# Optimization experiments

Measured on AMD Instinct MI355X. Metric: run time of the kernel, lower is better.

The kernel has to match this reference:

```python
import jax, jax.numpy as jnp
import numpy as np

N_NODES = 100000
N_EDGES = 1600000
D_IN, D_HID, D_OUT = 128, 128, 64


def setup_inputs() -> dict:
    key = jax.random.key(0)
    k1, k2, k3, k4 = jax.random.split(key, 4)
    x = jax.random.normal(k1, (N_NODES, D_IN), dtype=jnp.float32)
    edge_index = jax.random.randint(k2, (2, N_EDGES), 0, N_NODES, dtype=jnp.int64)
    # Glorot-style weights, zero bias (GCNConv defaults: weight + bias)
    W1 = jax.random.normal(k3, (D_IN, D_HID), dtype=jnp.float32) * (1.0 / np.sqrt(D_IN))
    b1 = jnp.zeros((D_HID,), dtype=jnp.float32)
    W2 = jax.random.normal(k4, (D_HID, D_OUT), dtype=jnp.float32) * (1.0 / np.sqrt(D_HID))
    b2 = jnp.zeros((D_OUT,), dtype=jnp.float32)
    return {"x": x, "edge_index": edge_index, "W1": W1, "b1": b1, "W2": W2, "b2": b2}


def reference(x, edge_index, W1, b1, W2, b2):
    n = x.shape[0]
    src, dst = edge_index[0], edge_index[1]
    # GCN symmetric normalization, add_self_loops=False
    ones = jnp.ones((src.shape[0],), dtype=x.dtype)
    deg = jax.ops.segment_sum(ones, dst, num_segments=n)
    deg_inv_sqrt = jnp.where(deg > 0, jax.lax.rsqrt(jnp.maximum(deg, 1.0)), 0.0)
    norm = deg_inv_sqrt[src] * deg_inv_sqrt[dst]  # [E]

    def gcn_conv(h, W, b):
        h = h @ W                                   # [N, d_out] transform first
        msg = h[src] * norm[:, None]                # [E, d_out] gather + scale
        agg = jax.ops.segment_sum(msg, dst, num_segments=n)  # scatter-add
        return agg + b

    h = jax.nn.relu(gcn_conv(x, W1, b1))
    # dropout(p=0.6) is identity in eval mode (training=False)
    return gcn_conv(h, W2, b2)
```

## Files before the change

kernel.cpp:

```cpp
#include <hip/hip_runtime.h>

#define N_NODES 100000
#define N_EDGES 1600000
#define NBUCK 391
#define CHUNKA 8192
#define NBLKA 196

typedef __bf16 bf16x8 __attribute__((ext_vector_type(8)));
typedef float f32x4 __attribute__((ext_vector_type(4)));

__device__ inline unsigned short bf1(float a) {
    unsigned u = __builtin_bit_cast(unsigned, a);
    u = (u + 0x7FFF + ((u >> 16) & 1)) >> 16;
    return (unsigned short)u;
}
__device__ inline unsigned bfpack(float a, float b) {
    unsigned ua = __builtin_bit_cast(unsigned, a);
    unsigned ub = __builtin_bit_cast(unsigned, b);
    ua = (ua + 0x7FFF + ((ua >> 16) & 1)) >> 16;
    ub = (ub + 0x7FFF + ((ub >> 16) & 1)) >> 16;
    return ua | (ub << 16);
}
__device__ inline float bf2f(unsigned short u) {
    return __builtin_bit_cast(float, ((unsigned)u) << 16);
}
__device__ inline float bflo(unsigned v) { return __builtin_bit_cast(float, v << 16); }
__device__ inline float bfhi(unsigned v) { return __builtin_bit_cast(float, v & 0xFFFF0000u); }

__global__ __launch_bounds__(256) void bhist_kernel(const int* __restrict__ ei,
                                                    int* __restrict__ bhist) {
    __shared__ int hist[NBUCK];
    const int t = threadIdx.x;
    const int e0 = blockIdx.x * CHUNKA;
    const int n  = min(CHUNKA, N_EDGES - e0);
    for (int i = t; i < NBUCK; i += 256) hist[i] = 0;
    __syncthreads();
    for (int i = t; i < n; i += 256) {
        int dst = ei[N_EDGES + e0 + i];
        atomicAdd(&hist[dst >> 8], 1);
    }
    __syncthreads();
    for (int i = t; i < NBUCK; i += 256)
        if (hist[i]) atomicAdd(&bhist[i], hist[i]);
}

__global__ __launch_bounds__(512) void prep_kernel(const int* __restrict__ bhist,
                                                   int* __restrict__ boffs,
                                                   const float* __restrict__ W1,
                                                   const float* __restrict__ W2,
                                                   unsigned short* __restrict__ Wt1,
                                                   unsigned short* __restrict__ Wt2) {
    const int t = threadIdx.x;
    if (blockIdx.x == 0) {
        __shared__ int s[512];
        int v = (t < NBUCK) ? bhist[t] : 0;
        s[t] = v;
        __syncthreads();
#pragma unroll
        for (int off = 1; off < 512; off <<= 1) {
            int tv = (t >= off) ? s[t - off] : 0;
            __syncthreads();
            s[t] += tv;
            __syncthreads();
        }
        if (t < NBUCK) boffs[t] = s[t] - v;
        if (t == NBUCK - 1) boffs[NBUCK] = s[t];
    } else if (blockIdx.x == 1) {
        for (int i = t; i < 128 * 128; i += 512) {
            int k = i >> 7, n = i & 127;
            Wt1[n * 128 + k] = bf1(W1[i]);
        }
    } else {
        for (int i = t; i < 128 * 64; i += 512) {
            int k = i >> 6, n = i & 63;
            Wt2[n * 128 + k] = bf1(W2[i]);
        }
    }
}

__global__ __launch_bounds__(256) void binA_kernel(const int* __restrict__ ei,
                                                   const int* __restrict__ boffs,
                                                   int* __restrict__ bcur,
                                                   unsigned* __restrict__ epk) {
    __shared__ int hist[NBUCK], base[NBUCK], cur[NBUCK];
    const int t = threadIdx.x;
    const int e0 = blockIdx.x * CHUNKA;
    const int n  = min(CHUNKA, N_EDGES - e0);
    for (int i = t; i < NBUCK; i += 256) hist[i] = 0;
    __syncthreads();
    for (int i = t; i < n; i += 256) {
        int dst = ei[N_EDGES + e0 + i];
        atomicAdd(&hist[dst >> 8], 1);
    }
    __syncthreads();
    for (int i = t; i < NBUCK; i += 256) {
        int h = hist[i];
        base[i] = boffs[i] + (h ? atomicAdd(&bcur[i], h) : 0);
        cur[i]  = 0;
    }
    __syncthreads();
    for (int i = t; i < n; i += 256) {
        int src = ei[e0 + i];
        int dst = ei[N_EDGES + e0 + i];
        int b   = dst >> 8;
        int r   = atomicAdd(&cur[b], 1);
        epk[base[b] + r] = ((unsigned)src << 8) | (unsigned)(dst & 255);
    }
}

__global__ __launch_bounds__(256) void binB_kernel(const unsigned* __restrict__ epk,
                                                   const int* __restrict__ boffs,
                                                   int* __restrict__ deg,
                                                   float* __restrict__ dis,
                                                   int* __restrict__ offs,
                                                   int* __restrict__ srcn) {
    __shared__ int cnt[256], s[256], loff[256];
    const int b  = blockIdx.x;
    const int t  = threadIdx.x;
    const int n0 = b << 8;
    const int base = boffs[b];
    const int end  = boffs[b + 1];
    cnt[t] = 0;
    __syncthreads();
    for (int e = base + t; e < end; e += 256)
        atomicAdd(&cnt[epk[e] & 255u], 1);
    __syncthreads();
    int v = cnt[t];
    s[t] = v;
    __syncthreads();
#pragma unroll
    for (int off = 1; off < 256; off <<= 1) {
        int tv = (t >= off) ? s[t - off] : 0;
        __syncthreads();
        s[t] += tv;
        __syncthreads();
    }
    loff[t] = s[t] - v;
    {
        int node = n0 + t;
        if (node < N_NODES) {
            deg[node]  = v;
            dis[node]  = (v > 0) ? rsqrtf((float)v) : 0.0f;
            offs[node] = base + loff[t];
        }
    }
    cnt[t] = 0;
    __syncthreads();
    for (int e = base + t; e < end; e += 256) {
        unsigned p = epk[e];
        int li  = (int)(p & 255u);
        int r   = atomicAdd(&cnt[li], 1);
        srcn[base + loff[li] + r] = (int)(p >> 8);
    }
}

__global__ __launch_bounds__(256) void gemm1_kernel(const float* __restrict__ x,
                                                    const unsigned short* __restrict__ Wt1,
                                                    const float* __restrict__ dis,
                                                    unsigned short* __restrict__ h1b) {
    __shared__ unsigned short Asm[64][136];
    __shared__ float diss[64];
    const int t = threadIdx.x;
    const int node0 = blockIdx.x * 64;

#pragma unroll
    for (int c = 0; c < 4; ++c) {
        int i = c * 256 + t;
        int row = i >> 4, ko = (i & 15) * 8;
        int gn = node0 + row;
        float4 v0 = make_float4(0, 0, 0, 0), v1 = v0;
        if (gn < N_NODES) {
            const float* p = x + (size_t)gn * 128 + ko;
            v0 = *(const float4*)p;
            v1 = *(const float4*)(p + 4);
        }
        uint4 o;
        o.x = bfpack(v0.x, v0.y); o.y = bfpack(v0.z, v0.w);
        o.z = bfpack(v1.x, v1.y); o.w = bfpack(v1.z, v1.w);
        *(uint4*)&Asm[row][ko] = o;
    }
    if (t < 64) {
        int gn = node0 + t;
        diss[t] = (gn < N_NODES) ? dis[gn] : 0.0f;
    }
    __syncthreads();

    const int wv = t >> 6, ln = t & 63;
    const int lc = ln & 15, q = ln >> 4;
    const int n0 = wv * 32;

    bf16x8 bfr[2][4];
#pragma unroll
    for (int nt = 0; nt < 2; ++nt)
#pragma unroll
        for (int k = 0; k < 4; ++k)
            bfr[nt][k] = *(const bf16x8*)(Wt1 + (size_t)(n0 + nt * 16 + lc) * 128 + k * 32 + q * 8);

    f32x4 acc[4][2];
#pragma unroll
    for (int m = 0; m < 4; ++m)
#pragma unroll
        for (int nt = 0; nt < 2; ++nt) acc[m][nt] = (f32x4)(0.0f);

#pragma unroll
    for (int k = 0; k < 4; ++k) {
        bf16x8 af[4];
#pragma unroll
        for (int m = 0; m < 4; ++m)
            af[m] = *(const bf16x8*)&Asm[m * 16 + lc][k * 32 + q * 8];
#pragma unroll
        for (int m = 0; m < 4; ++m)
#pragma unroll
            for (int nt = 0; nt < 2; ++nt)
                acc[m][nt] = __builtin_amdgcn_mfma_f32_16x16x32_bf16(af[m], bfr[nt][k], acc[m][nt], 0, 0, 0);
    }

#pragma unroll
    for (int m = 0; m < 4; ++m)
#pragma unroll
        for (int r = 0; r < 4; ++r) {
            int lr = m * 16 + q * 4 + r;
            int gn = node0 + lr;
            if (gn < N_NODES) {
                float dv = diss[lr];
#pragma unroll
                for (int nt = 0; nt < 2; ++nt)
                    h1b[(size_t)gn * 128 + n0 + nt * 16 + lc] = bf1(acc[m][nt][r] * dv);
            }
        }
}

__global__ __launch_bounds__(256) void agg1gemm2_kernel(const int* __restrict__ srcn,
                                                        const int* __restrict__ offs,
                                                        const int* __restrict__ deg,
                                                        const float* __restrict__ dis,
                                                        const unsigned short* __restrict__ h1b,
                                                        const float* __restrict__ b1,
                                                        const unsigned short* __restrict__ Wt2,
                                                        unsigned short* __restrict__ h2b) {
    __shared__ unsigned short Zs[64][136];
    __shared__ float diss[64];
    __shared__ int offs_s[64], deg_s[64];
    const int t = threadIdx.x;
    const int node0 = blockIdx.x * 64;
    if (t < 64) {
        int gn = node0 + t;
        bool ok = gn < N_NODES;
        offs_s[t] = ok ? offs[gn] : 0;
        deg_s[t]  = ok ? deg[gn] : 0;
        diss[t]   = ok ? dis[gn] : 0.0f;
    }
    __syncthreads();

    const int wv = t >> 6, ln = t & 63;
    const int qw = ln >> 4, lc = ln & 15;
    const uint4* __restrict__ h1q = (const uint4*)h1b;

    float4 bbA = *(const float4*)(b1 + lc * 8);
    float4 bbB = *(const float4*)(b1 + lc * 8 + 4);

#define ACC8(v)                                    \
    do {                                           \
        f0 += bflo((v).x); f1 += bfhi((v).x);      \
        f2 += bflo((v).y); f3 += bfhi((v).y);      \
        f4 += bflo((v).z); f5 += bfhi((v).z);      \
        f6 += bflo((v).w); f7 += bfhi((v).w);      \
    } while (0)

    for (int r = 0; r < 4; ++r) {
        const int lr  = wv * 16 + r * 4 + qw;
        const int beg = offs_s[lr];
        const int d   = deg_s[lr];
        float f0 = 0.f, f1 = 0.f, f2 = 0.f, f3 = 0.f,
              f4 = 0.f, f5 = 0.f, f6 = 0.f, f7 = 0.f;
        int k = 0;
        for (; k + 4 <= d; k += 4) {
            int s0 = srcn[beg + k];
            int s1 = srcn[beg + k + 1];
            int s2 = srcn[beg + k + 2];
            int s3 = srcn[beg + k + 3];
            uint4 v0 = h1q[(size_t)s0 * 16 + lc];
            uint4 v1 = h1q[(size_t)s1 * 16 + lc];
            uint4 v2 = h1q[(size_t)s2 * 16 + lc];
            uint4 v3 = h1q[(size_t)s3 * 16 + lc];
            ACC8(v0); ACC8(v1); ACC8(v2); ACC8(v3);
        }
        for (; k < d; ++k) {
            int s = srcn[beg + k];
            uint4 v = h1q[(size_t)s * 16 + lc];
            ACC8(v);
        }
        float dv = diss[lr];
        uint4 o;
        o.x = bfpack(fmaxf(dv * f0 + bbA.x, 0.0f), fmaxf(dv * f1 + bbA.y, 0.0f));
        o.y = bfpack(fmaxf(dv * f2 + bbA.z, 0.0f), fmaxf(dv * f3 + bbA.w, 0.0f));
        o.z = bfpack(fmaxf(dv * f4 + bbB.x, 0.0f), fmaxf(dv * f5 + bbB.y, 0.0f));
        o.w = bfpack(fmaxf(dv * f6 + bbB.z, 0.0f), fmaxf(dv * f7 + bbB.w, 0.0f));
        *(uint4*)&Zs[lr][lc * 8] = o;
    }
#undef ACC8
    __syncthreads();

    const int lc2 = ln & 15, q = ln >> 4;
    const int n0 = wv * 16;

    bf16x8 bfr[4];
#pragma unroll
    for (int k = 0; k < 4; ++k)
        bfr[k] = *(const bf16x8*)(Wt2 + (size_t)(n0 + lc2) * 128 + k * 32 + q * 8);

    f32x4 acc[4];
#pragma unroll
    for (int m = 0; m < 4; ++m) acc[m] = (f32x4)(0.0f);

#pragma unroll
    for (int k = 0; k < 4; ++k) {
        bf16x8 af[4];
#pragma unroll
        for (int m = 0; m < 4; ++m)
            af[m] = *(const bf16x8*)&Zs[m * 16 + lc2][k * 32 + q * 8];
#pragma unroll
        for (int m = 0; m < 4; ++m)
            acc[m] = __builtin_amdgcn_mfma_f32_16x16x32_bf16(af[m], bfr[k], acc[m], 0, 0, 0);
    }

#pragma unroll
    for (int m = 0; m < 4; ++m)
#pragma unroll
        for (int r = 0; r < 4; ++r) {
            int lr = m * 16 + q * 4 + r;
            int gn = node0 + lr;
            if (gn < N_NODES) {
                float dv = diss[lr];
                h2b[(size_t)gn * 64 + n0 + lc2] = bf1(acc[m][r] * dv);
            }
        }
}

__global__ __launch_bounds__(256) void agg2_kernel(const int* __restrict__ srcn,
                                                   const int* __restrict__ offs,
                                                   const int* __restrict__ deg,
                                                   const float* __restrict__ dis,
                                                   const unsigned short* __restrict__ h2b,
                                                   const float* __restrict__ b2,
                                                   float* __restrict__ out) {
    __shared__ float diss[64];
    __shared__ int offs_s[64], deg_s[64];
    const int t = threadIdx.x;
    const int node0 = blockIdx.x * 64;
    if (t < 64) {
        int gn = node0 + t;
        bool ok = gn < N_NODES;
        offs_s[t] = ok ? offs[gn] : 0;
        deg_s[t]  = ok ? deg[gn] : 0;
        diss[t]   = ok ? dis[gn] : 0.0f;
    }
    __syncthreads();

    const int wv = t >> 6, ln = t & 63;
    const int qw = ln >> 4, lc = ln & 15;
    const uint2* __restrict__ h2v = (const uint2*)h2b;

    float4 bb = *(const float4*)(b2 + lc * 4);

#define ACC4(v)                                    \
    do {                                           \
        f0 += bflo((v).x); f1 += bfhi((v).x);      \
        f2 += bflo((v).y); f3 += bfhi((v).y);      \
    } while (0)

    for (int r = 0; r < 4; ++r) {
        const int lr  = wv * 16 + r * 4 + qw;
        const int beg = offs_s[lr];
        const int d   = deg_s[lr];
        float f0 = 0.f, f1 = 0.f, f2 = 0.f, f3 = 0.f;
        int k = 0;
        for (; k + 4 <= d; k += 4) {
            int s0 = srcn[beg + k];
            int s1 = srcn[beg + k + 1];
            int s2 = srcn[beg + k + 2];
            int s3 = srcn[beg + k + 3];
            uint2 v0 = h2v[(size_t)s0 * 16 + lc];
            uint2 v1 = h2v[(size_t)s1 * 16 + lc];
            uint2 v2 = h2v[(size_t)s2 * 16 + lc];
            uint2 v3 = h2v[(size_t)s3 * 16 + lc];
            ACC4(v0); ACC4(v1); ACC4(v2); ACC4(v3);
        }
        for (; k < d; ++k) {
            int s = srcn[beg + k];
            uint2 v = h2v[(size_t)s * 16 + lc];
            ACC4(v);
        }
        int gn = node0 + lr;
        if (gn < N_NODES) {
            float dv = diss[lr];
            float4 o;
            o.x = dv * f0 + bb.x;
            o.y = dv * f1 + bb.y;
            o.z = dv * f2 + bb.z;
            o.w = dv * f3 + bb.w;
            *(float4*)(out + (size_t)gn * 64 + lc * 4) = o;
        }
    }
#undef ACC4
}

extern "C" void kernel_launch(void* const* d_in, const int* in_sizes, int n_in,
                              void* d_out, int out_size, void* d_ws, size_t ws_size,
                              hipStream_t stream) {
    const float* x  = (const float*)d_in[0];
    const int*   ei = (const int*)d_in[1];
    const float* W1 = (const float*)d_in[2];
    const float* b1 = (const float*)d_in[3];
    const float* W2 = (const float*)d_in[4];
    const float* b2 = (const float*)d_in[5];
    float* out = (float*)d_out;

    char* ws = (char*)d_ws;
    int*   bhist = (int*)(ws);
    int*   bcur  = (int*)(ws + (size_t)4 * 1024);
    int*   boffs = (int*)(ws + (size_t)8 * 1024);
    int*   deg   = (int*)(ws + (size_t)16 * 1024);
    int*   offs  = (int*)(ws + (size_t)512 * 1024);
    float* dis   = (float*)(ws + (size_t)1024 * 1024);
    unsigned short* Wt1 = (unsigned short*)(ws + (size_t)1536 * 1024);
    unsigned short* Wt2 = (unsigned short*)(ws + (size_t)1600 * 1024);
    unsigned* epk = (unsigned*)(ws + (size_t)2560 * 1024);
    int*   srcn  = (int*)(ws + (size_t)9216 * 1024);
    unsigned short* h1b = (unsigned short*)(ws + (size_t)16 * 1024 * 1024);
    unsigned short* h2b = (unsigned short*)(ws + (size_t)48 * 1024 * 1024);

    hipMemsetAsync(ws, 0, (size_t)8 * 1024, stream);

    bhist_kernel<<<NBLKA, 256, 0, stream>>>(ei, bhist);
    prep_kernel<<<3, 512, 0, stream>>>(bhist, boffs, W1, W2, Wt1, Wt2);
    binA_kernel<<<NBLKA, 256, 0, stream>>>(ei, boffs, bcur, epk);
    binB_kernel<<<NBUCK, 256, 0, stream>>>(epk, boffs, deg, dis, offs, srcn);
    gemm1_kernel<<<(N_NODES + 63) / 64, 256, 0, stream>>>(x, Wt1, dis, h1b);
    agg1gemm2_kernel<<<(N_NODES + 63) / 64, 256, 0, stream>>>(srcn, offs, deg, dis,
                                                              h1b, b1, Wt2, h2b);
    agg2_kernel<<<(N_NODES + 63) / 64, 256, 0, stream>>>(srcn, offs, deg, dis,
                                                         h2b, b2, out);
}
```

Measured before the change: 283.2 us.

## Replace two-pass bucket sort CSR build with global atomic degree count and scatter

```diff
diff --git a/kernel.cpp b/kernel.cpp
--- a/kernel.cpp
+++ b/kernel.cpp
@@ -21,14 +21,12 @@
     ub = (ub + 0x7FFF + ((ub >> 16) & 1)) >> 16;
     return ua | (ub << 16);
 }
-__device__ inline float bf2f(unsigned short u) {
-    return __builtin_bit_cast(float, ((unsigned)u) << 16);
-}
 __device__ inline float bflo(unsigned v) { return __builtin_bit_cast(float, v << 16); }
 __device__ inline float bfhi(unsigned v) { return __builtin_bit_cast(float, v & 0xFFFF0000u); }
 
-__global__ __launch_bounds__(256) void bhist_kernel(const int* __restrict__ ei,
-                                                    int* __restrict__ bhist) {
+__global__ __launch_bounds__(256) void hist_kernel(const int* __restrict__ ei,
+                                                   int* __restrict__ bhist,
+                                                   int* __restrict__ deg) {
     __shared__ int hist[NBUCK];
     const int t = threadIdx.x;
     const int e0 = blockIdx.x * CHUNKA;
@@ -38,6 +36,7 @@
     for (int i = t; i < n; i += 256) {
         int dst = ei[N_EDGES + e0 + i];
         atomicAdd(&hist[dst >> 8], 1);
+        atomicAdd(&deg[dst], 1);
     }
     __syncthreads();
     for (int i = t; i < NBUCK; i += 256)
@@ -78,54 +77,15 @@
     }
 }
 
-__global__ __launch_bounds__(256) void binA_kernel(const int* __restrict__ ei,
+__global__ __launch_bounds__(256) void offs_kernel(const int* __restrict__ deg,
                                                    const int* __restrict__ boffs,
-                                                   int* __restrict__ bcur,
-                                                   unsigned* __restrict__ epk) {
-    __shared__ int hist[NBUCK], base[NBUCK], cur[NBUCK];
-    const int t = threadIdx.x;
-    const int e0 = blockIdx.x * CHUNKA;
-    const int n  = min(CHUNKA, N_EDGES - e0);
-    for (int i = t; i < NBUCK; i += 256) hist[i] = 0;
-    __syncthreads();
-    for (int i = t; i < n; i += 256) {
-        int dst = ei[N_EDGES + e0 + i];
-        atomicAdd(&hist[dst >> 8], 1);
-    }
-    __syncthreads();
-    for (int i = t; i < NBUCK; i += 256) {
-        int h = hist[i];
-        base[i] = boffs[i] + (h ? atomicAdd(&bcur[i], h) : 0);
-        cur[i]  = 0;
-    }
-    __syncthreads();
-    for (int i = t; i < n; i += 256) {
-        int src = ei[e0 + i];
-        int dst = ei[N_EDGES + e0 + i];
-        int b   = dst >> 8;
-        int r   = atomicAdd(&cur[b], 1);
-        epk[base[b] + r] = ((unsigned)src << 8) | (unsigned)(dst & 255);
-    }
-}
-
-__global__ __launch_bounds__(256) void binB_kernel(const unsigned* __restrict__ epk,
-                                                   const int* __restrict__ boffs,
-                                                   int* __restrict__ deg,
+                                                   int* __restrict__ offs,
                                                    float* __restrict__ dis,
-                                                   int* __restrict__ offs,
-                                                   int* __restrict__ srcn) {
-    __shared__ int cnt[256], s[256], loff[256];
-    const int b  = blockIdx.x;
-    const int t  = threadIdx.x;
-    const int n0 = b << 8;
-    const int base = boffs[b];
-    const int end  = boffs[b + 1];
-    cnt[t] = 0;
-    __syncthreads();
-    for (int e = base + t; e < end; e += 256)
-        atomicAdd(&cnt[epk[e] & 255u], 1);
-    __syncthreads();
-    int v = cnt[t];
+                                                   int* __restrict__ cur) {
+    __shared__ int s[256];
+    const int b = blockIdx.x, t = threadIdx.x;
+    const int node = (b << 8) + t;
+    int v = (node < N_NODES) ? deg[node] : 0;
     s[t] = v;
     __syncthreads();
 #pragma unroll
@@ -135,22 +95,23 @@
         s[t] += tv;
         __syncthreads();
     }
-    loff[t] = s[t] - v;
-    {
-        int node = n0 + t;
-        if (node < N_NODES) {
-            deg[node]  = v;
-            dis[node]  = (v > 0) ? rsqrtf((float)v) : 0.0f;
-            offs[node] = base + loff[t];
-        }
-    }
-    cnt[t] = 0;
-    __syncthreads();
-    for (int e = base + t; e < end; e += 256) {
-        unsigned p = epk[e];
-        int li  = (int)(p & 255u);
-        int r   = atomicAdd(&cnt[li], 1);
-        srcn[base + loff[li] + r] = (int)(p >> 8);
+    if (node < N_NODES) {
+        offs[node] = boffs[b] + (s[t] - v);
+        dis[node]  = (v > 0) ? rsqrtf((float)v) : 0.0f;
+        cur[node]  = 0;
+    }
+}
+
+__global__ __launch_bounds__(256) void scatter_kernel(const int* __restrict__ ei,
+                                                      const int* __restrict__ offs,
+                                                      int* __restrict__ cur,
+                                                      int* __restrict__ srcn) {
+    int i = blockIdx.x * 256 + threadIdx.x;
+    if (i < N_EDGES) {
+        int src = ei[i];
+        int dst = ei[N_EDGES + i];
+        int r = atomicAdd(&cur[dst], 1);
+        srcn[offs[dst] + r] = src;
     }
 }
 
@@ -274,6 +235,26 @@
         float f0 = 0.f, f1 = 0.f, f2 = 0.f, f3 = 0.f,
               f4 = 0.f, f5 = 0.f, f6 = 0.f, f7 = 0.f;
         int k = 0;
+        for (; k + 8 <= d; k += 8) {
+            int s0 = srcn[beg + k];
+            int s1 = srcn[beg + k + 1];
+            int s2 = srcn[beg + k + 2];
+            int s3 = srcn[beg + k + 3];
+            int s4 = srcn[beg + k + 4];
+            int s5 = srcn[beg + k + 5];
+            int s6 = srcn[beg + k + 6];
+            int s7 = srcn[beg + k + 7];
+            uint4 v0 = h1q[(size_t)s0 * 16 + lc];
+            uint4 v1 = h1q[(size_t)s1 * 16 + lc];
+            uint4 v2 = h1q[(size_t)s2 * 16 + lc];
+            uint4 v3 = h1q[(size_t)s3 * 16 + lc];
+            uint4 v4 = h1q[(size_t)s4 * 16 + lc];
+            uint4 v5 = h1q[(size_t)s5 * 16 + lc];
+            uint4 v6 = h1q[(size_t)s6 * 16 + lc];
+            uint4 v7 = h1q[(size_t)s7 * 16 + lc];
+            ACC8(v0); ACC8(v1); ACC8(v2); ACC8(v3);
+            ACC8(v4); ACC8(v5); ACC8(v6); ACC8(v7);
+        }
         for (; k + 4 <= d; k += 4) {
             int s0 = srcn[beg + k];
             int s1 = srcn[beg + k + 1];
@@ -375,6 +356,26 @@
         const int d   = deg_s[lr];
         float f0 = 0.f, f1 = 0.f, f2 = 0.f, f3 = 0.f;
         int k = 0;
+        for (; k + 8 <= d; k += 8) {
+            int s0 = srcn[beg + k];
+            int s1 = srcn[beg + k + 1];
+            int s2 = srcn[beg + k + 2];
+            int s3 = srcn[beg + k + 3];
+            int s4 = srcn[beg + k + 4];
+            int s5 = srcn[beg + k + 5];
+            int s6 = srcn[beg + k + 6];
+            int s7 = srcn[beg + k + 7];
+            uint2 v0 = h2v[(size_t)s0 * 16 + lc];
+            uint2 v1 = h2v[(size_t)s1 * 16 + lc];
+            uint2 v2 = h2v[(size_t)s2 * 16 + lc];
+            uint2 v3 = h2v[(size_t)s3 * 16 + lc];
+            uint2 v4 = h2v[(size_t)s4 * 16 + lc];
+            uint2 v5 = h2v[(size_t)s5 * 16 + lc];
+            uint2 v6 = h2v[(size_t)s6 * 16 + lc];
+            uint2 v7 = h2v[(size_t)s7 * 16 + lc];
+            ACC4(v0); ACC4(v1); ACC4(v2); ACC4(v3);
+            ACC4(v4); ACC4(v5); ACC4(v6); ACC4(v7);
+        }
         for (; k + 4 <= d; k += 4) {
             int s0 = srcn[beg + k];
             int s1 = srcn[beg + k + 1];
@@ -418,24 +419,24 @@
 
     char* ws = (char*)d_ws;
     int*   bhist = (int*)(ws);
-    int*   bcur  = (int*)(ws + (size_t)4 * 1024);
     int*   boffs = (int*)(ws + (size_t)8 * 1024);
     int*   deg   = (int*)(ws + (size_t)16 * 1024);
-    int*   offs  = (int*)(ws + (size_t)512 * 1024);
-    float* dis   = (float*)(ws + (size_t)1024 * 1024);
-    unsigned short* Wt1 = (unsigned short*)(ws + (size_t)1536 * 1024);
-    unsigned short* Wt2 = (unsigned short*)(ws + (size_t)1600 * 1024);
-    unsigned* epk = (unsigned*)(ws + (size_t)2560 * 1024);
+    int*   cur   = (int*)(ws + (size_t)512 * 1024);
+    int*   offs  = (int*)(ws + (size_t)1024 * 1024);
+    float* dis   = (float*)(ws + (size_t)1536 * 1024);
+    unsigned short* Wt1 = (unsigned short*)(ws + (size_t)2048 * 1024);
+    unsigned short* Wt2 = (unsigned short*)(ws + (size_t)2112 * 1024);
     int*   srcn  = (int*)(ws + (size_t)9216 * 1024);
     unsigned short* h1b = (unsigned short*)(ws + (size_t)16 * 1024 * 1024);
     unsigned short* h2b = (unsigned short*)(ws + (size_t)48 * 1024 * 1024);
 
-    hipMemsetAsync(ws, 0, (size_t)8 * 1024, stream);
-
-    bhist_kernel<<<NBLKA, 256, 0, stream>>>(ei, bhist);
+    hipMemsetAsync(ws, 0, (size_t)12 * 1024, stream);
+    hipMemsetAsync(ws + (size_t)16 * 1024, 0, (size_t)400 * 1024, stream);
+
+    hist_kernel<<<NBLKA, 256, 0, stream>>>(ei, bhist, deg);
     prep_kernel<<<3, 512, 0, stream>>>(bhist, boffs, W1, W2, Wt1, Wt2);
-    binA_kernel<<<NBLKA, 256, 0, stream>>>(ei, boffs, bcur, epk);
-    binB_kernel<<<NBUCK, 256, 0, stream>>>(epk, boffs, deg, dis, offs, srcn);
+    offs_kernel<<<NBUCK, 256, 0, stream>>>(deg, boffs, offs, dis, cur);
+    scatter_kernel<<<(N_EDGES + 255) / 256, 256, 0, stream>>>(ei, offs, cur, srcn);
     gemm1_kernel<<<(N_NODES + 63) / 64, 256, 0, stream>>>(x, Wt1, dis, h1b);
     agg1gemm2_kernel<<<(N_NODES + 63) / 64, 256, 0, stream>>>(srcn, offs, deg, dis,
                                                               h1b, b1, Wt2, h2b);
```

Result: slower. 395.4 us (+39.6%).
